# Performance work log

Hardware: AMD Instinct MI355X
Metric: run time of the kernel (lower is better)

Reference implementation:

```python
import jax, jax.numpy as jnp
import numpy as np

HEAD = 12  # number of attention heads (init kwarg)


def setup_inputs() -> dict:
    key = jax.random.key(0)
    ks = jax.random.split(key, 6)
    B, N, F = 16, 1024, 768
    return {
        "x": jax.random.normal(ks[0], (B, N, F), dtype=jnp.float32),
        "wq": jax.random.normal(ks[1], (F,), dtype=jnp.float32),
        "bq": jnp.zeros((F,), dtype=jnp.float32),
        "wk": jax.random.normal(ks[2], (F,), dtype=jnp.float32),
        "bk": jnp.zeros((F,), dtype=jnp.float32),
        "wv": jax.random.normal(ks[3], (F,), dtype=jnp.float32),
        "bv": jnp.zeros((F,), dtype=jnp.float32),
        "wo": jax.random.normal(ks[4], (F,), dtype=jnp.float32),
        "bo": jnp.zeros((F,), dtype=jnp.float32),
    }


def reference(x, wq, bq, wk, bk, wv, bv, wo, bo):
    # x: [B, N, F]; depthwise (per-channel) q/k/v projections, MHSA, depthwise out proj
    B, N, F = x.shape
    d = F // HEAD
    scale = jnp.asarray(F, x.dtype) ** 0.5  # repo uses sqrt(feats), not sqrt(d_head)

    def to_heads(t):
        return t.reshape(B, N, HEAD, d)

    q = to_heads(x * wq + bq)  # [B, N, H, d]
    k = to_heads(x * wk + bk)
    v = to_heads(x * wv + bv)

    att = jnp.einsum("bqhd,bkhd->bhqk", q, k) / scale  # [B, H, N, N]
    att = jax.nn.softmax(att, axis=-1)
    o = jnp.einsum("bhqk,bkhd->bqhd", att, v).reshape(B, N, F)
    return o * wo + bo
```

## Files before the change

### kernel.cpp

```cpp
#include <hip/hip_runtime.h>
#include <hip/hip_bf16.h>
#include <cstdint>
#include <cstddef>

typedef __attribute__((ext_vector_type(8))) short short8;
typedef __attribute__((ext_vector_type(4))) short short4v;
typedef __attribute__((ext_vector_type(4))) float f32x4;
typedef __attribute__((ext_vector_type(16))) float f32x16;
typedef __attribute__((ext_vector_type(4))) unsigned int uint4v;

static constexpr int B_ = 16, N_ = 1024, F_ = 768, H_ = 12, D_ = 64;
static constexpr int NB = 64, NT = N_ / NB;
static constexpr int QB = 256;
static constexpr float RSCALE = 0.036084391824351615f;
static constexpr float QSCALE = 0.036084391824351615f * 1.4426950408889634f;
static constexpr float DEFER_THR = 8.0f;

__device__ __forceinline__ short f2bf(float f) {
    return __builtin_bit_cast(short, __float2bfloat16(f));
}
__device__ __forceinline__ unsigned cvtpk(float lo, float hi) {
    unsigned r;
    asm("v_cvt_pk_bf16_f32 %0, %1, %2" : "=v"(r) : "v"(lo), "v"(hi));
    return r;
}

#define GLB(p)  ((const __attribute__((address_space(1))) void*)(p))
#define LDSP(p) ((__attribute__((address_space(3))) void*)(p))

__global__ void __launch_bounds__(256) prep_kv(
    const float* __restrict__ x,
    const float* __restrict__ wk, const float* __restrict__ bk,
    const float* __restrict__ wv, const float* __restrict__ bv,
    short* __restrict__ Kt, short* __restrict__ Vt)
{
    const int bid = blockIdx.x;
    const int t   = bid & 15;
    const int bh  = bid >> 4;
    const int h   = bh % H_, b = bh / H_;
    const int nb  = t * NB;
    const int tid = threadIdx.x;
    short* Ktile = Kt + ((size_t)bid << 12);
    short* Vtile = Vt + ((size_t)bid << 12);

    {
        const int n = tid >> 2, sg = tid & 3;
        const float* xr  = x  + ((size_t)(b * N_ + nb + n)) * F_ + h * D_ + sg * 16;
        const float* wkp = wk + h * D_ + sg * 16;
        const float* bkp = bk + h * D_ + sg * 16;
        float xv[16];
        #pragma unroll
        for (int q = 0; q < 4; ++q) *(float4*)&xv[q * 4] = *(const float4*)(xr + q * 4);
        short kb[16];
        #pragma unroll
        for (int i = 0; i < 16; ++i) kb[i] = f2bf(xv[i] * wkp[i] + bkp[i]);
        const int swz = n & 7;
        #pragma unroll
        for (int c2 = 0; c2 < 2; ++c2) {
            const int c = sg * 2 + c2;
            *(short8*)&Ktile[n * 64 + ((c ^ swz) << 3)] = *(short8*)&kb[c2 * 8];
        }
    }
    {
        const int d = tid & 63, ng = tid >> 6;
        const float wvd = wv[h * D_ + d], bvd = bv[h * D_ + d];
        const float* xc = x + ((size_t)(b * N_ + nb + ng * 16)) * F_ + h * D_ + d;
        short vb[16];
        #pragma unroll
        for (int j = 0; j < 16; ++j) vb[j] = f2bf(xc[(size_t)j * F_] * wvd + bvd);
        const int swz = d & 7;
        #pragma unroll
        for (int c2 = 0; c2 < 2; ++c2) {
            const int c = ng * 2 + c2;
            *(short8*)&Vtile[d * 64 + ((c ^ swz) << 3)] = *(short8*)&vb[c2 * 8];
        }
    }
}

__global__ void __launch_bounds__(512, 4) attn_main(
    const float* __restrict__ x,
    const float* __restrict__ wq, const float* __restrict__ bq,
    const short* __restrict__ Kt, const short* __restrict__ Vt,
    const float* __restrict__ wo, const float* __restrict__ bo,
    float* __restrict__ out)
{
    __shared__ short KV[2][2][4096];

    const int tid  = threadIdx.x;
    const int w    = tid >> 6, lane = tid & 63;
    const int q32  = lane & 31, hi = lane >> 5;

    const int orig = blockIdx.x;
    const int sb   = (orig & 7) * 96 + (orig >> 3);
    const int qt   = sb & 3, bh = sb >> 2;
    const int h    = bh % H_, b = bh / H_;
    const int qrow0 = qt * QB + w * 32;
    const int qa    = qrow0 + q32;

    short8 qf[4];
    {
        const float* xq = x + ((size_t)(b * N_ + qa)) * F_ + h * D_;
        #pragma unroll
        for (int s = 0; s < 4; ++s) {
            const int ch0 = s * 16 + hi * 8;
            float4 a0 = *(const float4*)(xq + ch0);
            float4 a1 = *(const float4*)(xq + ch0 + 4);
            const float* wqp = wq + h * D_ + ch0;
            const float* bqp = bq + h * D_ + ch0;
            float q8[8] = {a0.x,a0.y,a0.z,a0.w,a1.x,a1.y,a1.z,a1.w};
            uint4v u;
            #pragma unroll
            for (int j = 0; j < 4; ++j) {
                const float lo = (q8[2*j]   * wqp[2*j]   + bqp[2*j])   * QSCALE;
                const float hf = (q8[2*j+1] * wqp[2*j+1] + bqp[2*j+1]) * QSCALE;
                u[j] = cvtpk(lo, hf);
            }
            qf[s] = __builtin_bit_cast(short8, u);
        }
    }

    const int swz = q32 & 7;
    int coff[4];
    #pragma unroll
    for (int s = 0; s < 4; ++s) coff[s] = (((s * 2 + hi) ^ swz) << 3);
    const int rA = q32 * 64;
    const int rB = (32 + q32) * 64;

    float m_ = -INFINITY, l_ = 0.f;
    f32x16 oA, oB;
    #pragma unroll
    for (int r = 0; r < 16; ++r) { oA[r] = 0.f; oB[r] = 0.f; }

    const size_t base = ((size_t)bh) * (NT * 4096);
    auto stage = [&](int buf, int tt) {
        const short* ks = Kt + base + ((size_t)tt << 12) + tid * 8;
        const short* vs = Vt + base + ((size_t)tt << 12) + tid * 8;
        __builtin_amdgcn_global_load_lds(GLB(ks), LDSP(&KV[buf][0][w * 512]), 16, 0, 0);
        __builtin_amdgcn_global_load_lds(GLB(vs), LDSP(&KV[buf][1][w * 512]), 16, 0, 0);
    };

    stage(0, 0);

    for (int t = 0; t < NT; ++t) {
        const int cur = t & 1;
        __syncthreads();
        if (t + 1 < NT) stage(cur ^ 1, t + 1);
        const short* Kb = &KV[cur][0][0];
        const short* Vb = &KV[cur][1][0];

        f32x16 sA, sB;
        #pragma unroll
        for (int r = 0; r < 16; ++r) { sA[r] = 0.f; sB[r] = 0.f; }
        __builtin_amdgcn_s_setprio(1);
        #pragma unroll
        for (int s = 0; s < 4; ++s) {
            short8 k0 = *(const short8*)&Kb[rA + coff[s]];
            short8 k1 = *(const short8*)&Kb[rB + coff[s]];
            sA = __builtin_amdgcn_mfma_f32_32x32x16_bf16(k0, qf[s], sA, 0, 0, 0);
            sB = __builtin_amdgcn_mfma_f32_32x32x16_bf16(k1, qf[s], sB, 0, 0, 0);
        }
        __builtin_amdgcn_s_setprio(0);

        float tm = sA[0];
        #pragma unroll
        for (int r = 1; r < 16; ++r) tm = fmaxf(tm, sA[r]);
        #pragma unroll
        for (int r = 0; r < 16; ++r) tm = fmaxf(tm, sB[r]);
        tm = fmaxf(tm, __shfl_xor(tm, 32, 64));

        if (!__all(tm - m_ <= DEFER_THR)) {
            const float mn = fmaxf(m_, tm);
            const float corr = exp2f(m_ - mn);
            l_ *= corr;
            #pragma unroll
            for (int r = 0; r < 16; ++r) { oA[r] *= corr; oB[r] *= corr; }
            m_ = mn;
        }

        float ps = 0.f;
        #pragma unroll
        for (int r = 0; r < 16; ++r) { sA[r] = exp2f(sA[r] - m_); ps += sA[r]; }
        #pragma unroll
        for (int r = 0; r < 16; ++r) { sB[r] = exp2f(sB[r] - m_); ps += sB[r]; }
        ps += __shfl_xor(ps, 32, 64);
        l_ += ps;

        short8 pf[4];
        {
            uint4v u0, u1, u2, u3;
            u0[0] = cvtpk(sA[0],  sA[1]);  u0[1] = cvtpk(sA[2],  sA[3]);
            u0[2] = cvtpk(sA[4],  sA[5]);  u0[3] = cvtpk(sA[6],  sA[7]);
            u1[0] = cvtpk(sA[8],  sA[9]);  u1[1] = cvtpk(sA[10], sA[11]);
            u1[2] = cvtpk(sA[12], sA[13]); u1[3] = cvtpk(sA[14], sA[15]);
            u2[0] = cvtpk(sB[0],  sB[1]);  u2[1] = cvtpk(sB[2],  sB[3]);
            u2[2] = cvtpk(sB[4],  sB[5]);  u2[3] = cvtpk(sB[6],  sB[7]);
            u3[0] = cvtpk(sB[8],  sB[9]);  u3[1] = cvtpk(sB[10], sB[11]);
            u3[2] = cvtpk(sB[12], sB[13]); u3[3] = cvtpk(sB[14], sB[15]);
            pf[0] = __builtin_bit_cast(short8, u0);
            pf[1] = __builtin_bit_cast(short8, u1);
            pf[2] = __builtin_bit_cast(short8, u2);
            pf[3] = __builtin_bit_cast(short8, u3);
        }

        __builtin_amdgcn_s_setprio(1);
        #pragma unroll
        for (int s = 0; s < 4; ++s) {
            const int cLo = ((2*s    ) ^ swz) << 3;
            const int cHi = ((2*s + 1) ^ swz) << 3;
            short4v aLo = *(const short4v*)&Vb[rA + cLo + 4*hi];
            short4v aHi = *(const short4v*)&Vb[rA + cHi + 4*hi];
            short4v bLo = *(const short4v*)&Vb[rB + cLo + 4*hi];
            short4v bHi = *(const short4v*)&Vb[rB + cHi + 4*hi];
            short8 v0 = {aLo[0],aLo[1],aLo[2],aLo[3], aHi[0],aHi[1],aHi[2],aHi[3]};
            short8 v1 = {bLo[0],bLo[1],bLo[2],bLo[3], bHi[0],bHi[1],bHi[2],bHi[3]};
            oA = __builtin_amdgcn_mfma_f32_32x32x16_bf16(v0, pf[s], oA, 0, 0, 0);
            oB = __builtin_amdgcn_mfma_f32_32x32x16_bf16(v1, pf[s], oB, 0, 0, 0);
        }
        __builtin_amdgcn_s_setprio(0);
    }

    const float invl = 1.f / l_;
    float* orow = out + ((size_t)(b * N_ + qa)) * F_;
    #pragma unroll
    for (int dsb = 0; dsb < 2; ++dsb) {
        #pragma unroll
        for (int j = 0; j < 4; ++j) {
            const int ch = h * D_ + dsb * 32 + 8 * j + 4 * hi;
            float4 wv = *(const float4*)(wo + ch);
            float4 bv = *(const float4*)(bo + ch);
            float4 o4;
            if (dsb == 0) {
                o4.x = oA[4*j+0] * invl * wv.x + bv.x;
                o4.y = oA[4*j+1] * invl * wv.y + bv.y;
                o4.z = oA[4*j+2] * invl * wv.z + bv.z;
                o4.w = oA[4*j+3] * invl * wv.w + bv.w;
            } else {
                o4.x = oB[4*j+0] * invl * wv.x + bv.x;
                o4.y = oB[4*j+1] * invl * wv.y + bv.y;
                o4.z = oB[4*j+2] * invl * wv.z + bv.z;
                o4.w = oB[4*j+3] * invl * wv.w + bv.w;
            }
            *(float4*)(orow + ch) = o4;
        }
    }
}

__global__ void __launch_bounds__(256) attn_fused(
    const float* __restrict__ x,
    const float* __restrict__ wq, const float* __restrict__ bq,
    const float* __restrict__ wk, const float* __restrict__ bk,
    const float* __restrict__ wv, const float* __restrict__ bv,
    const float* __restrict__ wo, const float* __restrict__ bo,
    float* __restrict__ out)
{
    __shared__ short Klds[64][72];
    __shared__ short Vt[64][72];
    __shared__ short Plds[4][16][72];

    const int tid = threadIdx.x;
    const int wave = tid >> 6, lane = tid & 63;
    const int g = lane >> 4, cc = lane & 15;
    const int bid = blockIdx.x;
    const int qt = bid & 15, t1 = bid >> 4;
    const int h = t1 % H_, b = t1 / H_;

    const int qrow = qt * 64 + wave * 16 + cc;
    const float* xq = x + ((size_t)(b * N_ + qrow)) * F_ + h * D_;
    short8 qf[2];
    #pragma unroll
    for (int kc = 0; kc < 2; ++kc) {
        const int dd = kc * 32 + g * 8;
        float4 a0 = *(const float4*)(xq + dd);
        float4 a1 = *(const float4*)(xq + dd + 4);
        float qa[8] = {a0.x,a0.y,a0.z,a0.w,a1.x,a1.y,a1.z,a1.w};
        #pragma unroll
        for (int i = 0; i < 8; ++i) {
            const int ch = h * D_ + dd + i;
            qf[kc][i] = f2bf((qa[i] * wq[ch] + bq[ch]) * RSCALE);
        }
    }
    const int srow = tid >> 2, seg = tid & 3;
    const int cb = h * D_ + seg * 16;
    float m_[4], l_[4];
    f32x4 oacc[4];
    #pragma unroll
    for (int r = 0; r < 4; ++r) { m_[r] = -INFINITY; l_[r] = 0.f; oacc[r] = (f32x4){0,0,0,0}; }

    for (int nb = 0; nb < N_; nb += 64) {
        __syncthreads();
        {
            const float* xr = x + ((size_t)(b * N_ + nb + srow)) * F_ + cb;
            float4 x0 = *(const float4*)(xr + 0), x1 = *(const float4*)(xr + 4);
            float4 x2 = *(const float4*)(xr + 8), x3 = *(const float4*)(xr + 12);
            float xf[16] = {x0.x,x0.y,x0.z,x0.w,x1.x,x1.y,x1.z,x1.w,
                            x2.x,x2.y,x2.z,x2.w,x3.x,x3.y,x3.z,x3.w};
            short8 k0, k1;
            #pragma unroll
            for (int i = 0; i < 8; ++i) {
                k0[i] = f2bf(xf[i] * wk[cb+i] + bk[cb+i]);
                k1[i] = f2bf(xf[i+8] * wk[cb+i+8] + bk[cb+i+8]);
            }
            *(short8*)&Klds[srow][seg*16] = k0;
            *(short8*)&Klds[srow][seg*16+8] = k1;
            #pragma unroll
            for (int i = 0; i < 16; ++i)
                Vt[seg*16+i][srow] = f2bf(xf[i] * wv[cb+i] + bv[cb+i]);
        }
        __syncthreads();
        f32x4 s[4];
        #pragma unroll
        for (int sub = 0; sub < 4; ++sub) {
            f32x4 acc = (f32x4){0,0,0,0};
            #pragma unroll
            for (int kc = 0; kc < 2; ++kc) {
                short8 kf = *(short8*)&Klds[sub*16+cc][kc*32+g*8];
                acc = __builtin_amdgcn_mfma_f32_16x16x32_bf16(qf[kc], kf, acc, 0,0,0);
            }
            s[sub] = acc;
        }
        float tm[4];
        #pragma unroll
        for (int r = 0; r < 4; ++r)
            tm[r] = fmaxf(fmaxf(s[0][r], s[1][r]), fmaxf(s[2][r], s[3][r]));
        #pragma unroll
        for (int r = 0; r < 4; ++r)
            #pragma unroll
            for (int off = 1; off < 16; off <<= 1)
                tm[r] = fmaxf(tm[r], __shfl_xor(tm[r], off, 64));
        float corr[4], ps[4];
        #pragma unroll
        for (int r = 0; r < 4; ++r) {
            float mn = fmaxf(m_[r], tm[r]);
            corr[r] = __expf(m_[r] - mn);
            m_[r] = mn; ps[r] = 0.f;
        }
        #pragma unroll
        for (int sub = 0; sub < 4; ++sub)
            #pragma unroll
            for (int r = 0; r < 4; ++r) {
                float p = __expf(s[sub][r] - m_[r]);
                s[sub][r] = p; ps[r] += p;
            }
        #pragma unroll
        for (int r = 0; r < 4; ++r) {
            #pragma unroll
            for (int off = 1; off < 16; off <<= 1)
                ps[r] += __shfl_xor(ps[r], off, 64);
            l_[r] = l_[r] * corr[r] + ps[r];
        }
        #pragma unroll
        for (int d = 0; d < 4; ++d)
            #pragma unroll
            for (int r = 0; r < 4; ++r) oacc[d][r] *= corr[r];
        #pragma unroll
        for (int sub = 0; sub < 4; ++sub)
            #pragma unroll
            for (int r = 0; r < 4; ++r)
                Plds[wave][g*4+r][sub*16+cc] = f2bf(s[sub][r]);
        short8 pf[2];
        #pragma unroll
        for (int nc = 0; nc < 2; ++nc)
            pf[nc] = *(short8*)&Plds[wave][cc][nc*32+g*8];
        #pragma unroll
        for (int d = 0; d < 4; ++d)
            #pragma unroll
            for (int nc = 0; nc < 2; ++nc) {
                short8 vf = *(short8*)&Vt[d*16+cc][nc*32+g*8];
                oacc[d] = __builtin_amdgcn_mfma_f32_16x16x32_bf16(pf[nc], vf, oacc[d], 0,0,0);
            }
    }
    #pragma unroll
    for (int r = 0; r < 4; ++r) l_[r] = 1.f / l_[r];
    const int orow0 = qt * 64 + wave * 16 + g * 4;
    #pragma unroll
    for (int d = 0; d < 4; ++d) {
        const int ch = h * D_ + d * 16 + cc;
        const float wov = wo[ch], bov = bo[ch];
        #pragma unroll
        for (int r = 0; r < 4; ++r)
            out[((size_t)(b * N_ + orow0 + r)) * F_ + ch] = oacc[d][r] * l_[r] * wov + bov;
    }
}

extern "C" void kernel_launch(void* const* d_in, const int* in_sizes, int n_in,
                              void* d_out, int out_size, void* d_ws, size_t ws_size,
                              hipStream_t stream) {
    const float* x  = (const float*)d_in[0];
    const float* wq = (const float*)d_in[1];
    const float* bq = (const float*)d_in[2];
    const float* wk = (const float*)d_in[3];
    const float* bk = (const float*)d_in[4];
    const float* wv = (const float*)d_in[5];
    const float* bv = (const float*)d_in[6];
    const float* wo = (const float*)d_in[7];
    const float* bo = (const float*)d_in[8];
    float* out = (float*)d_out;

    const size_t elems = (size_t)B_ * H_ * N_ * D_;
    const size_t need  = elems * 2 * 2;
    if (ws_size >= need) {
        short* Ktw = (short*)d_ws;
        short* Vtw = Ktw + elems;
        prep_kv<<<dim3(B_ * H_ * NT), dim3(256), 0, stream>>>(x, wk, bk, wv, bv, Ktw, Vtw);
        attn_main<<<dim3(B_ * H_ * (N_ / QB)), dim3(512), 0, stream>>>(
            x, wq, bq, Ktw, Vtw, wo, bo, out);
    } else {
        attn_fused<<<dim3(B_ * H_ * (N_ / 64)), dim3(256), 0, stream>>>(
            x, wq, bq, wk, bk, wv, bv, wo, bo, out);
    }
}
```

Before: 114.3 us.

## Halve query block to 4 waves and fold running max into MFMA accumulator init

Shrinks the query tile per block from 256 to 128 rows (256 threads, 4 waves), doubling the grid, and makes each wave stage two chunks of K and V per tile. The MFMA accumulators now start at -m so scores come out already max-shifted, which removes the per-element subtraction before exp2. Max and sum reductions become tree reductions, and exp2f is replaced by the raw hardware intrinsic. The smaller blocks add more K/V tile loads per query row and more blocks to schedule, in exchange for more independent blocks per CU and shorter dependency chains.

```diff
diff --git a/kernel.cpp b/kernel.cpp
--- a/kernel.cpp
+++ b/kernel.cpp
@@ -11,7 +11,7 @@
 
 static constexpr int B_ = 16, N_ = 1024, F_ = 768, H_ = 12, D_ = 64;
 static constexpr int NB = 64, NT = N_ / NB;
-static constexpr int QB = 256;
+static constexpr int QB = 128;
 static constexpr float RSCALE = 0.036084391824351615f;
 static constexpr float QSCALE = 0.036084391824351615f * 1.4426950408889634f;
 static constexpr float DEFER_THR = 8.0f;
@@ -77,7 +77,7 @@
     }
 }
 
-__global__ void __launch_bounds__(512, 4) attn_main(
+__global__ void __launch_bounds__(256, 4) attn_main(
     const float* __restrict__ x,
     const float* __restrict__ wq, const float* __restrict__ bq,
     const short* __restrict__ Kt, const short* __restrict__ Vt,
@@ -91,8 +91,8 @@
     const int q32  = lane & 31, hi = lane >> 5;
 
     const int orig = blockIdx.x;
-    const int sb   = (orig & 7) * 96 + (orig >> 3);
-    const int qt   = sb & 3, bh = sb >> 2;
+    const int sb   = (orig & 7) * 192 + (orig >> 3);
+    const int qt   = sb & 7, bh = sb >> 3;
     const int h    = bh % H_, b = bh / H_;
     const int qrow0 = qt * QB + w * 32;
     const int qa    = qrow0 + q32;
@@ -126,17 +126,19 @@
     const int rA = q32 * 64;
     const int rB = (32 + q32) * 64;
 
-    float m_ = -INFINITY, l_ = 0.f;
+    float m_ = 0.f, l_ = 0.f;
     f32x16 oA, oB;
     #pragma unroll
     for (int r = 0; r < 16; ++r) { oA[r] = 0.f; oB[r] = 0.f; }
 
     const size_t base = ((size_t)bh) * (NT * 4096);
     auto stage = [&](int buf, int tt) {
-        const short* ks = Kt + base + ((size_t)tt << 12) + tid * 8;
-        const short* vs = Vt + base + ((size_t)tt << 12) + tid * 8;
-        __builtin_amdgcn_global_load_lds(GLB(ks), LDSP(&KV[buf][0][w * 512]), 16, 0, 0);
-        __builtin_amdgcn_global_load_lds(GLB(vs), LDSP(&KV[buf][1][w * 512]), 16, 0, 0);
+        const short* tk = Kt + base + ((size_t)tt << 12) + w * 1024 + (lane << 3);
+        const short* tv = Vt + base + ((size_t)tt << 12) + w * 1024 + (lane << 3);
+        __builtin_amdgcn_global_load_lds(GLB(tk),       LDSP(&KV[buf][0][w*1024]),       16, 0, 0);
+        __builtin_amdgcn_global_load_lds(GLB(tk + 512), LDSP(&KV[buf][0][w*1024 + 512]), 16, 0, 0);
+        __builtin_amdgcn_global_load_lds(GLB(tv),       LDSP(&KV[buf][1][w*1024]),       16, 0, 0);
+        __builtin_amdgcn_global_load_lds(GLB(tv + 512), LDSP(&KV[buf][1][w*1024 + 512]), 16, 0, 0);
     };
 
     stage(0, 0);
@@ -148,9 +150,10 @@
         const short* Kb = &KV[cur][0][0];
         const short* Vb = &KV[cur][1][0];
 
+        const float negm = -m_;
         f32x16 sA, sB;
         #pragma unroll
-        for (int r = 0; r < 16; ++r) { sA[r] = 0.f; sB[r] = 0.f; }
+        for (int r = 0; r < 16; ++r) { sA[r] = negm; sB[r] = negm; }
         __builtin_amdgcn_s_setprio(1);
         #pragma unroll
         for (int s = 0; s < 4; ++s) {
@@ -161,41 +164,55 @@
         }
         __builtin_amdgcn_s_setprio(0);
 
-        float tm = sA[0];
-        #pragma unroll
-        for (int r = 1; r < 16; ++r) tm = fmaxf(tm, sA[r]);
-        #pragma unroll
-        for (int r = 0; r < 16; ++r) tm = fmaxf(tm, sB[r]);
-        tm = fmaxf(tm, __shfl_xor(tm, 32, 64));
-
-        if (!__all(tm - m_ <= DEFER_THR)) {
-            const float mn = fmaxf(m_, tm);
-            const float corr = exp2f(m_ - mn);
+        float mx[16];
+        #pragma unroll
+        for (int r = 0; r < 16; ++r) mx[r] = fmaxf(sA[r], sB[r]);
+        #pragma unroll
+        for (int off = 8; off > 0; off >>= 1) {
+            #pragma unroll
+            for (int i = 0; i < 8; ++i)
+                if (i < off) mx[i] = fmaxf(mx[i], mx[i + off]);
+        }
+        const float tm = fmaxf(mx[0], __shfl_xor(mx[0], 32, 64));
+
+        if (!__all(tm <= DEFER_THR)) {
+            const float corr = __builtin_amdgcn_exp2f(-tm);
             l_ *= corr;
             #pragma unroll
             for (int r = 0; r < 16; ++r) { oA[r] *= corr; oB[r] *= corr; }
-            m_ = mn;
-        }
-
-        float ps = 0.f;
-        #pragma unroll
-        for (int r = 0; r < 16; ++r) { sA[r] = exp2f(sA[r] - m_); ps += sA[r]; }
-        #pragma unroll
-        for (int r = 0; r < 16; ++r) { sB[r] = exp2f(sB[r] - m_); ps += sB[r]; }
-        ps += __shfl_xor(ps, 32, 64);
-        l_ += ps;
+            #pragma unroll
+            for (int r = 0; r < 16; ++r) { sA[r] -= tm; sB[r] -= tm; }
+            m_ += tm;
+        }
+
+        float e[32];
+        #pragma unroll
+        for (int r = 0; r < 16; ++r) {
+            e[r]      = __builtin_amdgcn_exp2f(sA[r]);
+            e[16 + r] = __builtin_amdgcn_exp2f(sB[r]);
+        }
+        float su[16];
+        #pragma unroll
+        for (int i = 0; i < 16; ++i) su[i] = e[i] + e[i + 16];
+        #pragma unroll
+        for (int off = 8; off > 0; off >>= 1) {
+            #pragma unroll
+            for (int i = 0; i < 8; ++i)
+                if (i < off) su[i] += su[i + off];
+        }
+        l_ += su[0] + __shfl_xor(su[0], 32, 64);
 
         short8 pf[4];
         {
             uint4v u0, u1, u2, u3;
-            u0[0] = cvtpk(sA[0],  sA[1]);  u0[1] = cvtpk(sA[2],  sA[3]);
-            u0[2] = cvtpk(sA[4],  sA[5]);  u0[3] = cvtpk(sA[6],  sA[7]);
-            u1[0] = cvtpk(sA[8],  sA[9]);  u1[1] = cvtpk(sA[10], sA[11]);
-            u1[2] = cvtpk(sA[12], sA[13]); u1[3] = cvtpk(sA[14], sA[15]);
-            u2[0] = cvtpk(sB[0],  sB[1]);  u2[1] = cvtpk(sB[2],  sB[3]);
-            u2[2] = cvtpk(sB[4],  sB[5]);  u2[3] = cvtpk(sB[6],  sB[7]);
-            u3[0] = cvtpk(sB[8],  sB[9]);  u3[1] = cvtpk(sB[10], sB[11]);
-            u3[2] = cvtpk(sB[12], sB[13]); u3[3] = cvtpk(sB[14], sB[15]);
+            u0[0] = cvtpk(e[0],  e[1]);  u0[1] = cvtpk(e[2],  e[3]);
+            u0[2] = cvtpk(e[4],  e[5]);  u0[3] = cvtpk(e[6],  e[7]);
+            u1[0] = cvtpk(e[8],  e[9]);  u1[1] = cvtpk(e[10], e[11]);
+            u1[2] = cvtpk(e[12], e[13]); u1[3] = cvtpk(e[14], e[15]);
+            u2[0] = cvtpk(e[16], e[17]); u2[1] = cvtpk(e[18], e[19]);
+            u2[2] = cvtpk(e[20], e[21]); u2[3] = cvtpk(e[22], e[23]);
+            u3[0] = cvtpk(e[24], e[25]); u3[1] = cvtpk(e[26], e[27]);
+            u3[2] = cvtpk(e[28], e[29]); u3[3] = cvtpk(e[30], e[31]);
             pf[0] = __builtin_bit_cast(short8, u0);
             pf[1] = __builtin_bit_cast(short8, u1);
             pf[2] = __builtin_bit_cast(short8, u2);
@@ -402,7 +419,7 @@
         short* Ktw = (short*)d_ws;
         short* Vtw = Ktw + elems;
         prep_kv<<<dim3(B_ * H_ * NT), dim3(256), 0, stream>>>(x, wk, bk, wv, bv, Ktw, Vtw);
-        attn_main<<<dim3(B_ * H_ * (N_ / QB)), dim3(512), 0, stream>>>(
+        attn_main<<<dim3(B_ * H_ * (N_ / QB)), dim3(256), 0, stream>>>(
             x, wq, bq, Ktw, Vtw, wo, bo, out);
     } else {
         attn_fused<<<dim3(B_ * H_ * (N_ / 64)), dim3(256), 0, stream>>>(
```

Result: faster. 101.1 us (-11.5%).
